# Kernel tuning notes

Measured on AMD Instinct MI355X. Metric: run time of the kernel, lower is better.

## Reference

```python
import jax, jax.numpy as jnp
import numpy as np


def setup_inputs() -> dict:
    key = jax.random.key(0)
    X = jax.random.normal(key, (8, 4096, 64), dtype=jnp.float32)
    return {"X": X}


def reference(X) -> jnp.ndarray:
    # raw_weights: [B, S, S] = X @ X^T
    raw_weights = jnp.einsum("bsd,btd->bst", X, X)
    # softmax over last (key) dim, as in F.softmax(raw_weights, dim=2)
    weights = jax.nn.softmax(raw_weights, axis=2)
    # y: [B, S, D]
    y = jnp.einsum("bst,btd->bsd", weights, X).astype(jnp.float32)
    return y
```

## Files before the change

### kernel.cpp

```cpp
#include <hip/hip_runtime.h>
#include <hip/hip_bf16.h>
#include <stdint.h>


#define BB 8
#define SS 4096
#define DD 64
#define KVB 64
#define LDK 72

typedef __attribute__((ext_vector_type(8))) _Float16 f16x8;
typedef __attribute__((ext_vector_type(4))) _Float16 f16x4;
typedef __attribute__((ext_vector_type(2))) __fp16 h16x2;
typedef __attribute__((ext_vector_type(8))) __bf16 bf16x8;
typedef __attribute__((ext_vector_type(4))) float f32x4;

__device__ __forceinline__ _Float16 f2h(float f) { return (_Float16)f; }
__device__ __forceinline__ __bf16 f2bf(float f) { return (__bf16)f; }
__device__ __forceinline__ float exp2g(float x) { return __builtin_amdgcn_exp2f(x); }

__device__ __forceinline__ void gload_lds16(const _Float16* g, _Float16* l) {
  __builtin_amdgcn_global_load_lds(
      (const __attribute__((address_space(1))) uint32_t*)g,
      (__attribute__((address_space(3))) uint32_t*)l, 16, 0, 0);
}

__global__ __launch_bounds__(256)
void prepack(const float* __restrict__ X, _Float16* __restrict__ Gh,
             _Float16* __restrict__ Gl, _Float16* __restrict__ Gt) {
  const int b  = blockIdx.x >> 6;
  const int s0 = (blockIdx.x & 63) * 64;
  const int t  = threadIdx.x;
  const int r  = t >> 2;
  const int cq = t & 3;

  __shared__ float Xs[64][68];

  {
    const float* src = X + ((size_t)b * SS + s0 + r) * DD + cq * 16;
    float4 f0 = ((const float4*)src)[0];
    float4 f1 = ((const float4*)src)[1];
    float4 f2 = ((const float4*)src)[2];
    float4 f3 = ((const float4*)src)[3];
    *(float4*)&Xs[r][cq * 16 + 0]  = f0;
    *(float4*)&Xs[r][cq * 16 + 4]  = f1;
    *(float4*)&Xs[r][cq * 16 + 8]  = f2;
    *(float4*)&Xs[r][cq * 16 + 12] = f3;
  }
  __syncthreads();

  const size_t rowbase = ((size_t)b * SS + s0 + r) * DD;
#pragma unroll
  for (int cc = 0; cc < 2; ++cc) {
    const int c = cq * 2 + cc;
    f16x8 h, lo;
#pragma unroll
    for (int j = 0; j < 8; ++j) {
      float v = Xs[r][c * 8 + j];
      _Float16 hv = f2h(v);
      h[j]  = hv;
      lo[j] = f2h(v - (float)hv);
    }
    const int csw = c ^ (r & 7);
    *(f16x8*)(Gh + rowbase + csw * 8) = h;
    *(f16x8*)(Gl + rowbase + csw * 8) = lo;
  }

  const size_t tbase = ((size_t)b * DD + r) * SS + s0;
#pragma unroll
  for (int cc = 0; cc < 2; ++cc) {
    const int c  = cq * 2 + cc;
    const int g  = c >> 2;
    const int qt = c & 3;
    f16x8 h;
#pragma unroll
    for (int j = 0; j < 8; ++j) {
      const int kvl = 32 * g + 16 * (j >> 2) + 4 * qt + (j & 3);
      h[j] = f2h(Xs[kvl][r]);
    }
    const int csw = c ^ (r & 7);
    *(f16x8*)(Gt + tbase + csw * 8) = h;
  }
}

template <int NSPLIT>
__global__ __launch_bounds__(256, 4)
void attn_fwd8(float* __restrict__ Y, const _Float16* __restrict__ Gh,
               const _Float16* __restrict__ Gl, const _Float16* __restrict__ Gt,
               _Float16* __restrict__ Opart, float* __restrict__ ML) {
  const int b    = blockIdx.x & 7;
  const int q0   = ((blockIdx.x >> 3) & 63) * 64;
  const int half = (NSPLIT == 2) ? (blockIdx.x >> 9) : 0;
  const int kvbase = half * (SS / NSPLIT);
  const int NT2    = (SS / NSPLIT) / KVB;

  const int tid  = threadIdx.x;
  const int wid  = tid >> 6;
  const int lane = tid & 63;
  const int lrow = lane & 15;
  const int qt   = lane >> 4;
  const int key  = lane & 7;

  __shared__ __align__(16) _Float16 Kh[2][KVB][DD];
  __shared__ __align__(16) _Float16 Vt[2][DD][KVB];

  const _Float16* GhB = Gh + (size_t)b * SS * DD;
  const _Float16* GlB = Gl + (size_t)b * SS * DD;
  const _Float16* GtB = Gt + (size_t)b * DD * SS;

  const int chA = (qt ^ key) * 8;
  const int chB = ((4 + qt) ^ key) * 8;

  const float LOG2E = 1.4426950408889634f;
  f16x8 qf[2];
  float msum = 0.f;
  {
    const int s = q0 + wid * 16 + lrow;
    const _Float16* rh = GhB + (size_t)s * DD;
    const _Float16* rl = GlB + (size_t)s * DD;
#pragma unroll
    for (int kd = 0; kd < 2; ++kd) {
      const int ch = kd ? chB : chA;
      f16x8 h  = *(const f16x8*)(rh + ch);
      f16x8 lo = *(const f16x8*)(rl + ch);
#pragma unroll
      for (int j = 0; j < 8; ++j) {
        float q = (float)h[j] + (float)lo[j];
        msum += q * q;
        qf[kd][j] = f2h(q * LOG2E);
      }
    }
  }
  msum += __shfl_xor(msum, 16);
  msum += __shfl_xor(msum, 32);
  const float m = LOG2E * msum;
  const f32x4 minit = {-m, -m, -m, -m};

  f16x8 ones;
#pragma unroll
  for (int j = 0; j < 8; ++j) ones[j] = (_Float16)1.0f;

  f32x4 sumacc = {0.f, 0.f, 0.f, 0.f};
  f32x4 accO[4];
#pragma unroll
  for (int dt = 0; dt < 4; ++dt)
#pragma unroll
    for (int r = 0; r < 4; ++r) accO[dt][r] = 0.f;

  const int lr8 = lane >> 3;
  const int co  = (lane & 7) * 8;

  auto stage = [&](int t, int bufi) {
    const int kv0 = kvbase + t * KVB;
#pragma unroll
    for (int i = 0; i < 2; ++i) {
      const int r0 = wid * 16 + i * 8;
      const int gr = kv0 + r0 + lr8;
      gload_lds16(GhB + (size_t)gr * DD + co, &Kh[bufi][r0][0]);
      gload_lds16(GtB + (size_t)(r0 + lr8) * SS + kv0 + co, &Vt[bufi][r0][0]);
    }
  };

  stage(0, 0);
  __syncthreads();

  for (int t = 0; t < NT2; ++t) {
    const int buf = t & 1;
    if (t + 1 < NT2) stage(t + 1, buf ^ 1);

    f32x4 S[4];

    __builtin_amdgcn_s_setprio(1);
#pragma unroll
    for (int s = 0; s < 4; ++s) {
      const int row = s * 16 + lrow;
      f16x8 a0 = *(const f16x8*)&Kh[buf][row][chA];
      f16x8 a1 = *(const f16x8*)&Kh[buf][row][chB];
      S[s] = __builtin_amdgcn_mfma_f32_16x16x32_f16(a0, qf[0], minit, 0, 0, 0);
      S[s] = __builtin_amdgcn_mfma_f32_16x16x32_f16(a1, qf[1], S[s], 0, 0, 0);
    }
    __builtin_amdgcn_s_setprio(0);

#pragma unroll
    for (int s = 0; s < 4; ++s) {
      f32x4 p;
#pragma unroll
      for (int r = 0; r < 4; ++r) p[r] = exp2g(S[s][r]);
      S[s] = p;
    }

    union { f16x8 v; h16x2 h[4]; } pb0u, pb1u;
    pb0u.h[0] = __builtin_amdgcn_cvt_pkrtz(S[0][0], S[0][1]);
    pb0u.h[1] = __builtin_amdgcn_cvt_pkrtz(S[0][2], S[0][3]);
    pb0u.h[2] = __builtin_amdgcn_cvt_pkrtz(S[1][0], S[1][1]);
    pb0u.h[3] = __builtin_amdgcn_cvt_pkrtz(S[1][2], S[1][3]);
    pb1u.h[0] = __builtin_amdgcn_cvt_pkrtz(S[2][0], S[2][1]);
    pb1u.h[1] = __builtin_amdgcn_cvt_pkrtz(S[2][2], S[2][3]);
    pb1u.h[2] = __builtin_amdgcn_cvt_pkrtz(S[3][0], S[3][1]);
    pb1u.h[3] = __builtin_amdgcn_cvt_pkrtz(S[3][2], S[3][3]);

    __builtin_amdgcn_s_setprio(1);
    sumacc = __builtin_amdgcn_mfma_f32_16x16x32_f16(ones, pb0u.v, sumacc, 0, 0, 0);
    sumacc = __builtin_amdgcn_mfma_f32_16x16x32_f16(ones, pb1u.v, sumacc, 0, 0, 0);

#pragma unroll
    for (int dt = 0; dt < 4; ++dt) {
      const _Float16* vr = &Vt[buf][dt * 16 + lrow][0];
      f16x8 av0 = *(const f16x8*)(vr + chA);
      f16x8 av1 = *(const f16x8*)(vr + chB);
      accO[dt] = __builtin_amdgcn_mfma_f32_16x16x32_f16(av0, pb0u.v, accO[dt], 0, 0, 0);
      accO[dt] = __builtin_amdgcn_mfma_f32_16x16x32_f16(av1, pb1u.v, accO[dt], 0, 0, 0);
    }
    __builtin_amdgcn_s_setprio(0);

    __syncthreads();
  }

  const float lsum = sumacc[0];

  const int srow = q0 + wid * 16 + lrow;
  if (NSPLIT == 1) {
    const float inv = 1.f / lsum;
    float* Yr = Y + ((size_t)b * SS + srow) * DD;
#pragma unroll
    for (int dt = 0; dt < 4; ++dt)
#pragma unroll
      for (int r = 0; r < 4; ++r)
        Yr[dt * 16 + qt * 4 + r] = accO[dt][r] * inv;
  } else {
    _Float16* Or = Opart + (((size_t)half * BB + b) * SS + srow) * DD;
#pragma unroll
    for (int dt = 0; dt < 4; ++dt) {
      f16x4 o4;
#pragma unroll
      for (int r = 0; r < 4; ++r) o4[r] = f2h(accO[dt][r]);
      *(f16x4*)(Or + dt * 16 + qt * 4) = o4;
    }
    if (qt == 0) {
      float* mlr = ML + (((size_t)half * BB + b) * SS + srow) * 2;
      mlr[0] = m;
      mlr[1] = lsum;
    }
  }
}

__global__ __launch_bounds__(256)
void combine2(float* __restrict__ Y, const _Float16* __restrict__ Opart,
              const float* __restrict__ ML) {
  const size_t NROW = (size_t)BB * SS;
  const int tid = threadIdx.x;
  const size_t row = (size_t)blockIdx.x * 32 + (tid >> 3);
  const int d0 = (tid & 7) * 8;

  const float m0 = ML[row * 2 + 0];
  const float l0 = ML[row * 2 + 1];
  const float m1 = ML[(NROW + row) * 2 + 0];
  const float l1 = ML[(NROW + row) * 2 + 1];
  const float M  = fmaxf(m0, m1);
  const float w0 = exp2g(m0 - M);
  const float w1 = exp2g(m1 - M);
  const float inv = 1.f / (w0 * l0 + w1 * l1);

  f16x8 a = *(const f16x8*)(Opart + row * DD + d0);
  f16x8 c = *(const f16x8*)(Opart + (NROW + row) * DD + d0);
  float* y = Y + row * DD + d0;
#pragma unroll
  for (int h = 0; h < 2; ++h) {
    float4 o;
    o.x = (w0 * (float)a[h * 4 + 0] + w1 * (float)c[h * 4 + 0]) * inv;
    o.y = (w0 * (float)a[h * 4 + 1] + w1 * (float)c[h * 4 + 1]) * inv;
    o.z = (w0 * (float)a[h * 4 + 2] + w1 * (float)c[h * 4 + 2]) * inv;
    o.w = (w0 * (float)a[h * 4 + 3] + w1 * (float)c[h * 4 + 3]) * inv;
    ((float4*)y)[h] = o;
  }
}

__global__ __launch_bounds__(256, 2)
void attn_fwd_r2(const float* __restrict__ X, float* __restrict__ Y) {
  const int nqb = SS / 64;
  const int b  = blockIdx.x / nqb;
  const int q0 = (blockIdx.x % nqb) * 64;
  const int tid  = threadIdx.x;
  const int wid  = tid >> 6;
  const int lane = tid & 63;
  const int lrow = lane & 15;
  const int lhi  = lane >> 4;

  __shared__ __align__(16) __bf16 Xh[KVB][LDK];
  __shared__ __align__(16) __bf16 Xl[KVB][LDK];
  __shared__ __align__(16) __bf16 XT[DD][LDK];
  __shared__ __align__(16) __bf16 Pl[4][16][LDK];

  const float* Xb = X + (size_t)b * SS * DD;

  bf16x8 qh[2], ql[2];
  {
    const float* qp = Xb + (size_t)(q0 + wid * 16 + lrow) * DD;
#pragma unroll
    for (int kk = 0; kk < 2; ++kk) {
      const float4* p = reinterpret_cast<const float4*>(qp + kk * 32 + lhi * 8);
      float4 f0 = p[0], f1 = p[1];
      float v[8] = {f0.x, f0.y, f0.z, f0.w, f1.x, f1.y, f1.z, f1.w};
      bf16x8 h, lo;
#pragma unroll
      for (int j = 0; j < 8; ++j) {
        __bf16 hv = f2bf(v[j]);
        h[j]  = hv;
        lo[j] = f2bf(v[j] - (float)hv);
      }
      qh[kk] = h;
      ql[kk] = lo;
    }
  }

  float m[4], lsum[4];
  f32x4 accO[4];
#pragma unroll
  for (int r = 0; r < 4; ++r) { m[r] = -INFINITY; lsum[r] = 0.f; }
#pragma unroll
  for (int c = 0; c < 4; ++c)
#pragma unroll
    for (int r = 0; r < 4; ++r) accO[c][r] = 0.f;

  for (int kv0 = 0; kv0 < SS; kv0 += KVB) {
    __syncthreads();
    {
      const int r  = tid >> 2;
      const int c0 = (tid & 3) * 16;
      const float* src = Xb + (size_t)(kv0 + r) * DD + c0;
#pragma unroll
      for (int half = 0; half < 2; ++half) {
        const float4* p = reinterpret_cast<const float4*>(src + half * 8);
        float4 f0 = p[0], f1 = p[1];
        float v[8] = {f0.x, f0.y, f0.z, f0.w, f1.x, f1.y, f1.z, f1.w};
        bf16x8 h, lo;
#pragma unroll
        for (int j = 0; j < 8; ++j) {
          __bf16 hv = f2bf(v[j]);
          h[j]  = hv;
          lo[j] = f2bf(v[j] - (float)hv);
        }
        *reinterpret_cast<bf16x8*>(&Xh[r][c0 + half * 8]) = h;
        *reinterpret_cast<bf16x8*>(&Xl[r][c0 + half * 8]) = lo;
#pragma unroll
        for (int j = 0; j < 8; ++j) XT[c0 + half * 8 + j][r] = h[j];
      }
    }
    __syncthreads();

    f32x4 Sacc[4];
#pragma unroll
    for (int c = 0; c < 4; ++c)
#pragma unroll
      for (int r = 0; r < 4; ++r) Sacc[c][r] = 0.f;

#pragma unroll
    for (int kk = 0; kk < 2; ++kk) {
#pragma unroll
      for (int c = 0; c < 4; ++c) {
        bf16x8 bh = *reinterpret_cast<bf16x8*>(&Xh[c * 16 + lrow][kk * 32 + lhi * 8]);
        bf16x8 bl = *reinterpret_cast<bf16x8*>(&Xl[c * 16 + lrow][kk * 32 + lhi * 8]);
        Sacc[c] = __builtin_amdgcn_mfma_f32_16x16x32_bf16(qh[kk], bh, Sacc[c], 0, 0, 0);
        Sacc[c] = __builtin_amdgcn_mfma_f32_16x16x32_bf16(qh[kk], bl, Sacc[c], 0, 0, 0);
        Sacc[c] = __builtin_amdgcn_mfma_f32_16x16x32_bf16(ql[kk], bh, Sacc[c], 0, 0, 0);
      }
    }

#pragma unroll
    for (int r = 0; r < 4; ++r) {
      float v = fmaxf(fmaxf(Sacc[0][r], Sacc[1][r]), fmaxf(Sacc[2][r], Sacc[3][r]));
#pragma unroll
      for (int off = 1; off < 16; off <<= 1)
        v = fmaxf(v, __shfl_xor(v, off, 16));
      const float mnew  = fmaxf(m[r], v);
      const float scale = __expf(m[r] - mnew);
      m[r] = mnew;

      float rowsum = 0.f;
#pragma unroll
      for (int c = 0; c < 4; ++c) {
        float p = __expf(Sacc[c][r] - mnew);
        rowsum += p;
        Pl[wid][lhi * 4 + r][c * 16 + lrow] = f2bf(p);
      }
#pragma unroll
      for (int off = 1; off < 16; off <<= 1)
        rowsum += __shfl_xor(rowsum, off, 16);

      lsum[r] = lsum[r] * scale + rowsum;
#pragma unroll
      for (int c = 0; c < 4; ++c) accO[c][r] *= scale;
    }
    __syncthreads();

#pragma unroll
    for (int kk = 0; kk < 2; ++kk) {
      bf16x8 pa = *reinterpret_cast<bf16x8*>(&Pl[wid][lrow][kk * 32 + lhi * 8]);
#pragma unroll
      for (int c = 0; c < 4; ++c) {
        bf16x8 vb = *reinterpret_cast<bf16x8*>(&XT[c * 16 + lrow][kk * 32 + lhi * 8]);
        accO[c] = __builtin_amdgcn_mfma_f32_16x16x32_bf16(pa, vb, accO[c], 0, 0, 0);
      }
    }
  }

  float* Yb = Y + (size_t)b * SS * DD;
  const int rowbase = q0 + wid * 16;
#pragma unroll
  for (int r = 0; r < 4; ++r) {
    const float inv = 1.f / lsum[r];
#pragma unroll
    for (int c = 0; c < 4; ++c) {
      Yb[(size_t)(rowbase + lhi * 4 + r) * DD + c * 16 + lrow] = accO[c][r] * inv;
    }
  }
}

extern "C" void kernel_launch(void* const* d_in, const int* in_sizes, int n_in,
                              void* d_out, int out_size, void* d_ws, size_t ws_size,
                              hipStream_t stream) {
  const float* X = (const float*)d_in[0];
  float* Y = (float*)d_out;

  const size_t elems   = (size_t)BB * SS * DD;
  const size_t packB   = 3 * elems * sizeof(_Float16);
  const size_t opartB  = 2 * elems * sizeof(_Float16);
  const size_t mlB     = 2 * (size_t)BB * SS * 2 * sizeof(float);
  const size_t needSplit = packB + opartB + mlB;

  if (ws_size >= needSplit) {
    _Float16* Gh = (_Float16*)d_ws;
    _Float16* Gl = Gh + elems;
    _Float16* Gt = Gl + elems;
    _Float16* Opart = (_Float16*)((char*)d_ws + packB);
    float* ML = (float*)((char*)d_ws + packB + opartB);
    prepack<<<dim3(BB * 64), dim3(256), 0, stream>>>(X, Gh, Gl, Gt);
    attn_fwd8<2><<<dim3(2 * BB * (SS / 64)), dim3(256), 0, stream>>>(
        Y, Gh, Gl, Gt, Opart, ML);
    combine2<<<dim3((BB * SS) / 32), dim3(256), 0, stream>>>(Y, Opart, ML);
  } else if (ws_size >= packB) {
    _Float16* Gh = (_Float16*)d_ws;
    _Float16* Gl = Gh + elems;
    _Float16* Gt = Gl + elems;
    prepack<<<dim3(BB * 64), dim3(256), 0, stream>>>(X, Gh, Gl, Gt);
    attn_fwd8<1><<<dim3(BB * (SS / 64)), dim3(256), 0, stream>>>(
        Y, Gh, Gl, Gt, nullptr, nullptr);
  } else {
    attn_fwd_r2<<<dim3(BB * (SS / 64)), dim3(256), 0, stream>>>(X, Y);
  }
}
```

Baseline: 109.5 us.

## Process two 16-row query sub-tiles per wave to reuse K/V fragments

Each block now covers 128 query rows instead of 64, and each wave handles two 16-row query sub-tiles. Every K and V fragment read from LDS feeds two MFMA chains, which halves LDS traffic and global K/V staging per query row. The price is double the accumulator and score registers, so launch bounds drop from 4 to 2 blocks per CU. The grid also has half as many blocks (512 with the split), which lowers occupancy and latency hiding.

```diff
diff --git a/kernel.cpp b/kernel.cpp
--- a/kernel.cpp
+++ b/kernel.cpp
@@ -84,13 +84,13 @@
 }
 
 template <int NSPLIT>
-__global__ __launch_bounds__(256, 4)
-void attn_fwd8(float* __restrict__ Y, const _Float16* __restrict__ Gh,
+__global__ __launch_bounds__(256, 2)
+void attn_fwd9(float* __restrict__ Y, const _Float16* __restrict__ Gh,
                const _Float16* __restrict__ Gl, const _Float16* __restrict__ Gt,
                _Float16* __restrict__ Opart, float* __restrict__ ML) {
-  const int b    = blockIdx.x & 7;
-  const int q0   = ((blockIdx.x >> 3) & 63) * 64;
-  const int half = (NSPLIT == 2) ? (blockIdx.x >> 9) : 0;
+  const int b     = blockIdx.x & 7;
+  const int q0    = ((blockIdx.x >> 3) & 31) * 128;
+  const int half  = (NSPLIT == 2) ? (blockIdx.x >> 8) : 0;
   const int kvbase = half * (SS / NSPLIT);
   const int NT2    = (SS / NSPLIT) / KVB;
 
@@ -112,12 +112,15 @@
   const int chB = ((4 + qt) ^ key) * 8;
 
   const float LOG2E = 1.4426950408889634f;
-  f16x8 qf[2];
-  float msum = 0.f;
-  {
-    const int s = q0 + wid * 16 + lrow;
+  f16x8 qf[2][2];
+  f32x4 minit[2];
+  float mke[2];
+#pragma unroll
+  for (int qs = 0; qs < 2; ++qs) {
+    const int s = q0 + wid * 32 + qs * 16 + lrow;
     const _Float16* rh = GhB + (size_t)s * DD;
     const _Float16* rl = GlB + (size_t)s * DD;
+    float msum = 0.f;
 #pragma unroll
     for (int kd = 0; kd < 2; ++kd) {
       const int ch = kd ? chB : chA;
@@ -127,25 +130,28 @@
       for (int j = 0; j < 8; ++j) {
         float q = (float)h[j] + (float)lo[j];
         msum += q * q;
-        qf[kd][j] = f2h(q * LOG2E);
-      }
-    }
-  }
-  msum += __shfl_xor(msum, 16);
-  msum += __shfl_xor(msum, 32);
-  const float m = LOG2E * msum;
-  const f32x4 minit = {-m, -m, -m, -m};
+        qf[qs][kd][j] = f2h(q * LOG2E);
+      }
+    }
+    msum += __shfl_xor(msum, 16);
+    msum += __shfl_xor(msum, 32);
+    const float m = LOG2E * msum;
+    mke[qs] = m;
+    minit[qs] = f32x4{-m, -m, -m, -m};
+  }
 
   f16x8 ones;
 #pragma unroll
   for (int j = 0; j < 8; ++j) ones[j] = (_Float16)1.0f;
 
-  f32x4 sumacc = {0.f, 0.f, 0.f, 0.f};
-  f32x4 accO[4];
-#pragma unroll
-  for (int dt = 0; dt < 4; ++dt)
-#pragma unroll
-    for (int r = 0; r < 4; ++r) accO[dt][r] = 0.f;
+  f32x4 sumacc[2] = {{0.f, 0.f, 0.f, 0.f}, {0.f, 0.f, 0.f, 0.f}};
+  f32x4 accO[2][4];
+#pragma unroll
+  for (int qs = 0; qs < 2; ++qs)
+#pragma unroll
+    for (int dt = 0; dt < 4; ++dt)
+#pragma unroll
+      for (int r = 0; r < 4; ++r) accO[qs][dt][r] = 0.f;
 
   const int lr8 = lane >> 3;
   const int co  = (lane & 7) * 8;
@@ -168,7 +174,7 @@
     const int buf = t & 1;
     if (t + 1 < NT2) stage(t + 1, buf ^ 1);
 
-    f32x4 S[4];
+    f32x4 S[2][4];
 
     __builtin_amdgcn_s_setprio(1);
 #pragma unroll
@@ -176,70 +182,83 @@
       const int row = s * 16 + lrow;
       f16x8 a0 = *(const f16x8*)&Kh[buf][row][chA];
       f16x8 a1 = *(const f16x8*)&Kh[buf][row][chB];
-      S[s] = __builtin_amdgcn_mfma_f32_16x16x32_f16(a0, qf[0], minit, 0, 0, 0);
-      S[s] = __builtin_amdgcn_mfma_f32_16x16x32_f16(a1, qf[1], S[s], 0, 0, 0);
+#pragma unroll
+      for (int qs = 0; qs < 2; ++qs) {
+        S[qs][s] = __builtin_amdgcn_mfma_f32_16x16x32_f16(a0, qf[qs][0], minit[qs], 0, 0, 0);
+        S[qs][s] = __builtin_amdgcn_mfma_f32_16x16x32_f16(a1, qf[qs][1], S[qs][s], 0, 0, 0);
+      }
     }
     __builtin_amdgcn_s_setprio(0);
 
-#pragma unroll
-    for (int s = 0; s < 4; ++s) {
-      f32x4 p;
-#pragma unroll
-      for (int r = 0; r < 4; ++r) p[r] = exp2g(S[s][r]);
-      S[s] = p;
-    }
-
-    union { f16x8 v; h16x2 h[4]; } pb0u, pb1u;
-    pb0u.h[0] = __builtin_amdgcn_cvt_pkrtz(S[0][0], S[0][1]);
-    pb0u.h[1] = __builtin_amdgcn_cvt_pkrtz(S[0][2], S[0][3]);
-    pb0u.h[2] = __builtin_amdgcn_cvt_pkrtz(S[1][0], S[1][1]);
-    pb0u.h[3] = __builtin_amdgcn_cvt_pkrtz(S[1][2], S[1][3]);
-    pb1u.h[0] = __builtin_amdgcn_cvt_pkrtz(S[2][0], S[2][1]);
-    pb1u.h[1] = __builtin_amdgcn_cvt_pkrtz(S[2][2], S[2][3]);
-    pb1u.h[2] = __builtin_amdgcn_cvt_pkrtz(S[3][0], S[3][1]);
-    pb1u.h[3] = __builtin_amdgcn_cvt_pkrtz(S[3][2], S[3][3]);
+    union { f16x8 v; h16x2 h[4]; } pb[2][2];
+#pragma unroll
+    for (int qs = 0; qs < 2; ++qs) {
+#pragma unroll
+      for (int s = 0; s < 4; ++s) {
+        f32x4 p;
+#pragma unroll
+        for (int r = 0; r < 4; ++r) p[r] = exp2g(S[qs][s][r]);
+        S[qs][s] = p;
+      }
+      pb[qs][0].h[0] = __builtin_amdgcn_cvt_pkrtz(S[qs][0][0], S[qs][0][1]);
+      pb[qs][0].h[1] = __builtin_amdgcn_cvt_pkrtz(S[qs][0][2], S[qs][0][3]);
+      pb[qs][0].h[2] = __builtin_amdgcn_cvt_pkrtz(S[qs][1][0], S[qs][1][1]);
+      pb[qs][0].h[3] = __builtin_amdgcn_cvt_pkrtz(S[qs][1][2], S[qs][1][3]);
+      pb[qs][1].h[0] = __builtin_amdgcn_cvt_pkrtz(S[qs][2][0], S[qs][2][1]);
+      pb[qs][1].h[1] = __builtin_amdgcn_cvt_pkrtz(S[qs][2][2], S[qs][2][3]);
+      pb[qs][1].h[2] = __builtin_amdgcn_cvt_pkrtz(S[qs][3][0], S[qs][3][1]);
+      pb[qs][1].h[3] = __builtin_amdgcn_cvt_pkrtz(S[qs][3][2], S[qs][3][3]);
+    }
 
     __builtin_amdgcn_s_setprio(1);
-    sumacc = __builtin_amdgcn_mfma_f32_16x16x32_f16(ones, pb0u.v, sumacc, 0, 0, 0);
-    sumacc = __builtin_amdgcn_mfma_f32_16x16x32_f16(ones, pb1u.v, sumacc, 0, 0, 0);
+#pragma unroll
+    for (int qs = 0; qs < 2; ++qs) {
+      sumacc[qs] = __builtin_amdgcn_mfma_f32_16x16x32_f16(ones, pb[qs][0].v, sumacc[qs], 0, 0, 0);
+      sumacc[qs] = __builtin_amdgcn_mfma_f32_16x16x32_f16(ones, pb[qs][1].v, sumacc[qs], 0, 0, 0);
+    }
 
 #pragma unroll
     for (int dt = 0; dt < 4; ++dt) {
       const _Float16* vr = &Vt[buf][dt * 16 + lrow][0];
       f16x8 av0 = *(const f16x8*)(vr + chA);
       f16x8 av1 = *(const f16x8*)(vr + chB);
-      accO[dt] = __builtin_amdgcn_mfma_f32_16x16x32_f16(av0, pb0u.v, accO[dt], 0, 0, 0);
-      accO[dt] = __builtin_amdgcn_mfma_f32_16x16x32_f16(av1, pb1u.v, accO[dt], 0, 0, 0);
+#pragma unroll
+      for (int qs = 0; qs < 2; ++qs) {
+        accO[qs][dt] = __builtin_amdgcn_mfma_f32_16x16x32_f16(av0, pb[qs][0].v, accO[qs][dt], 0, 0, 0);
+        accO[qs][dt] = __builtin_amdgcn_mfma_f32_16x16x32_f16(av1, pb[qs][1].v, accO[qs][dt], 0, 0, 0);
+      }
     }
     __builtin_amdgcn_s_setprio(0);
 
     __syncthreads();
   }
 
-  const float lsum = sumacc[0];
-
-  const int srow = q0 + wid * 16 + lrow;
-  if (NSPLIT == 1) {
-    const float inv = 1.f / lsum;
-    float* Yr = Y + ((size_t)b * SS + srow) * DD;
-#pragma unroll
-    for (int dt = 0; dt < 4; ++dt)
-#pragma unroll
-      for (int r = 0; r < 4; ++r)
-        Yr[dt * 16 + qt * 4 + r] = accO[dt][r] * inv;
-  } else {
-    _Float16* Or = Opart + (((size_t)half * BB + b) * SS + srow) * DD;
-#pragma unroll
-    for (int dt = 0; dt < 4; ++dt) {
-      f16x4 o4;
-#pragma unroll
-      for (int r = 0; r < 4; ++r) o4[r] = f2h(accO[dt][r]);
-      *(f16x4*)(Or + dt * 16 + qt * 4) = o4;
-    }
-    if (qt == 0) {
-      float* mlr = ML + (((size_t)half * BB + b) * SS + srow) * 2;
-      mlr[0] = m;
-      mlr[1] = lsum;
+#pragma unroll
+  for (int qs = 0; qs < 2; ++qs) {
+    const float lsum = sumacc[qs][0];
+    const int srow = q0 + wid * 32 + qs * 16 + lrow;
+    if (NSPLIT == 1) {
+      const float inv = 1.f / lsum;
+      float* Yr = Y + ((size_t)b * SS + srow) * DD;
+#pragma unroll
+      for (int dt = 0; dt < 4; ++dt)
+#pragma unroll
+        for (int r = 0; r < 4; ++r)
+          Yr[dt * 16 + qt * 4 + r] = accO[qs][dt][r] * inv;
+    } else {
+      _Float16* Or = Opart + (((size_t)half * BB + b) * SS + srow) * DD;
+#pragma unroll
+      for (int dt = 0; dt < 4; ++dt) {
+        f16x4 o4;
+#pragma unroll
+        for (int r = 0; r < 4; ++r) o4[r] = f2h(accO[qs][dt][r]);
+        *(f16x4*)(Or + dt * 16 + qt * 4) = o4;
+      }
+      if (qt == 0) {
+        float* mlr = ML + (((size_t)half * BB + b) * SS + srow) * 2;
+        mlr[0] = mke[qs];
+        mlr[1] = lsum;
+      }
     }
   }
 }
@@ -435,7 +454,7 @@
     _Float16* Opart = (_Float16*)((char*)d_ws + packB);
     float* ML = (float*)((char*)d_ws + packB + opartB);
     prepack<<<dim3(BB * 64), dim3(256), 0, stream>>>(X, Gh, Gl, Gt);
-    attn_fwd8<2><<<dim3(2 * BB * (SS / 64)), dim3(256), 0, stream>>>(
+    attn_fwd9<2><<<dim3(2 * BB * (SS / 128)), dim3(256), 0, stream>>>(
         Y, Gh, Gl, Gt, Opart, ML);
     combine2<<<dim3((BB * SS) / 32), dim3(256), 0, stream>>>(Y, Opart, ML);
   } else if (ws_size >= packB) {
@@ -443,7 +462,7 @@
     _Float16* Gl = Gh + elems;
     _Float16* Gt = Gl + elems;
     prepack<<<dim3(BB * 64), dim3(256), 0, stream>>>(X, Gh, Gl, Gt);
-    attn_fwd8<1><<<dim3(BB * (SS / 64)), dim3(256), 0, stream>>>(
+    attn_fwd9<1><<<dim3(BB * (SS / 128)), dim3(256), 0, stream>>>(
         Y, Gh, Gl, Gt, nullptr, nullptr);
   } else {
     attn_fwd_r2<<<dim3(BB * (SS / 64)), dim3(256), 0, stream>>>(X, Y);
```

Result: no change. 108.9 us (-0.6%).
